# Kernel tuning notes

Measured on AMD Instinct MI355X. Metric: run time of the kernel, lower is better.

Reference implementation:

```python
import jax, jax.numpy as jnp
import numpy as np

N_NODES = 100000
N_EDGES = 1600000
IN_FEATS = 256
OUT_FEATS = 64


def setup_inputs() -> dict:
    key = jax.random.key(0)
    k1, k2, k3, k4 = jax.random.split(key, 4)
    feat = jax.random.normal(k1, (N_NODES, IN_FEATS), dtype=jnp.float32)
    # Glorot uniform init for weight
    limit = float(np.sqrt(6.0 / (IN_FEATS + OUT_FEATS)))
    weight = jax.random.uniform(k2, (IN_FEATS, OUT_FEATS), dtype=jnp.float32,
                                minval=-limit, maxval=limit)
    bias = jnp.zeros((OUT_FEATS,), dtype=jnp.float32)
    src = jax.random.randint(k3, (N_EDGES,), 0, N_NODES, dtype=jnp.int32)
    dst = jax.random.randint(k4, (N_EDGES,), 0, N_NODES, dtype=jnp.int32)
    return {"feat": feat, "weight": weight, "bias": bias, "src": src, "dst": dst}


def reference(feat, weight, bias, src, dst):
    N = feat.shape[0]
    ones = jnp.ones(src.shape[0], dtype=feat.dtype)
    # degrees for symmetric ('both') GCN normalization, clamped to >= 1
    deg_out = jnp.maximum(jax.ops.segment_sum(ones, src, num_segments=N), 1.0)
    deg_in = jnp.maximum(jax.ops.segment_sum(ones, dst, num_segments=N), 1.0)
    norm_out = jax.lax.rsqrt(deg_out)  # [N]
    norm_in = jax.lax.rsqrt(deg_in)    # [N]
    # in_feats > out_feats: project first, then aggregate (forward's taken branch)
    h = jnp.matmul(feat, weight) * norm_out[:, None]          # [N, out]
    agg = jax.ops.segment_sum(h[src], dst, num_segments=N)    # gather+scatter SpMM
    rst = agg * norm_in[:, None] + bias
    return jax.nn.relu(rst)
```

## Files before the change

kernel.cpp:

```cpp
#include <hip/hip_runtime.h>

#define N_NODES 100000
#define N_EDGES 1600000
#define IN_F 256
#define OUT_F 64
#define NPAD 100096
#define NB 391
#define NBLK 512
#define CHUNK 3125
#define MSIZE (2*NB*NBLK)
#define SC_BLOCKS 1564
#define CAP 12288

typedef __attribute__((ext_vector_type(8))) _Float16 half8v;
typedef __attribute__((ext_vector_type(4))) float f32x4;

__device__ __forceinline__ unsigned short f2bf(float f) {
    unsigned u = __builtin_bit_cast(unsigned, f);
    return (unsigned short)((u + 0x7FFFu + ((u >> 16) & 1u)) >> 16);
}
__device__ __forceinline__ float bf2f(unsigned s) {
    return __builtin_bit_cast(float, s << 16);
}
__device__ __forceinline__ half8v cvt8(float4 x, float4 y) {
    half8v r;
    r[0] = (_Float16)x.x; r[1] = (_Float16)x.y; r[2] = (_Float16)x.z; r[3] = (_Float16)x.w;
    r[4] = (_Float16)y.x; r[5] = (_Float16)y.y; r[6] = (_Float16)y.z; r[7] = (_Float16)y.w;
    return r;
}

__global__ __launch_bounds__(256) void histA_kernel(const int* __restrict__ src,
                                                    const int* __restrict__ dst,
                                                    int* __restrict__ hist_g,
                                                    const float* __restrict__ W,
                                                    _Float16* __restrict__ Wt2) {
    __shared__ int hD[NB], hS[NB];
    int b = blockIdx.x, t = threadIdx.x;
    if (b < 64) {
        int i = b * 256 + t;
        int k = i >> 6, c = i & 63;
        int ks4 = k >> 5, kin = k & 31, l4v = kin >> 3, kq = kin & 7;
        int cf  = c >> 4, l15v = c & 15;
        size_t idx = (((size_t)(ks4 * 4 + cf) * 64) + l4v * 16 + l15v) * 8 + kq;
        Wt2[idx] = (_Float16)W[i];
    }
    for (int j = t; j < NB; j += 256) { hD[j] = 0; hS[j] = 0; }
    __syncthreads();
    int e0 = b * CHUNK;
    for (int e = e0 + t; e < e0 + CHUNK; e += 256) {
        atomicAdd(&hD[dst[e] >> 8], 1);
        atomicAdd(&hS[src[e] >> 8], 1);
    }
    __syncthreads();
    for (int j = t; j < NB; j += 256) {
        hist_g[j * NBLK + b] = hD[j];
        hist_g[NB * NBLK + j * NBLK + b] = hS[j];
    }
}

__global__ __launch_bounds__(256) void scan1_kernel(int* __restrict__ data,
                                                    int* __restrict__ partials) {
    __shared__ int sm[256];
    int i = blockIdx.x * 256 + threadIdx.x;
    int v = (i < MSIZE) ? data[i] : 0;
    sm[threadIdx.x] = v;
    __syncthreads();
    int x = v;
    #pragma unroll
    for (int off = 1; off < 256; off <<= 1) {
        int tv = 0;
        if ((int)threadIdx.x >= off) tv = sm[threadIdx.x - off];
        __syncthreads();
        x += tv;
        sm[threadIdx.x] = x;
        __syncthreads();
    }
    if (i < MSIZE) data[i] = x - v;
    if (threadIdx.x == 255) partials[blockIdx.x] = x;
}

__global__ __launch_bounds__(1024) void scan2_kernel(int* __restrict__ partials) {
    __shared__ int sm[1024];
    int i = threadIdx.x;
    int v0 = (2 * i     < SC_BLOCKS) ? partials[2 * i]     : 0;
    int v1 = (2 * i + 1 < SC_BLOCKS) ? partials[2 * i + 1] : 0;
    int pv = v0 + v1;
    sm[i] = pv;
    __syncthreads();
    int x = pv;
    #pragma unroll
    for (int off = 1; off < 1024; off <<= 1) {
        int tv = (i >= off) ? sm[i - off] : 0;
        __syncthreads();
        x += tv;
        sm[i] = x;
        __syncthreads();
    }
    int excl = x - pv;
    if (2 * i     < SC_BLOCKS) partials[2 * i]     = excl;
    if (2 * i + 1 < SC_BLOCKS) partials[2 * i + 1] = excl + v0;
}

__device__ __forceinline__ int gscan(const int* __restrict__ hist_g,
                                     const int* __restrict__ partials, int idx) {
    return hist_g[idx] + partials[idx >> 8];
}

__global__ __launch_bounds__(256) void part_kernel(const int* __restrict__ src,
                                                   const int* __restrict__ dst,
                                                   const int* __restrict__ hist_g,
                                                   const int* __restrict__ partials,
                                                   unsigned* __restrict__ edge_buf,
                                                   int* __restrict__ src_part) {
    __shared__ unsigned stageA[CHUNK], stageB[CHUNK];
    __shared__ unsigned short bkt[CHUNK];
    __shared__ int L[512], cur[512];
    __shared__ int baseD[NB], baseS[NB];
    const int b = blockIdx.x, t = threadIdx.x;
    const int e0 = b * CHUNK;

    for (int j = t; j < NB; j += 256) {
        baseD[j] = gscan(hist_g, partials, j * NBLK + b);
        baseS[j] = gscan(hist_g, partials, NB * NBLK + j * NBLK + b) - N_EDGES;
    }

    L[t] = 0; L[t + 256] = 0;
    __syncthreads();
    for (int i = t; i < CHUNK; i += 256) {
        int d = dst[e0 + i];
        stageA[i] = (unsigned)d;
        atomicAdd(&L[d >> 8], 1);
    }
    __syncthreads();
    int v0 = L[t], v1 = L[t + 256];
    #pragma unroll
    for (int off = 1; off < 512; off <<= 1) {
        int a0 = (t >= off) ? L[t - off] : 0;
        int a1 = (t + 256 >= off) ? L[t + 256 - off] : 0;
        __syncthreads();
        L[t] += a0; L[t + 256] += a1;
        __syncthreads();
    }
    {
        int i0 = L[t], i1 = L[t + 256];
        __syncthreads();
        L[t] = i0 - v0;  L[t + 256] = i1 - v1;
        cur[t] = i0 - v0; cur[t + 256] = i1 - v1;
    }
    __syncthreads();
    for (int i = t; i < CHUNK; i += 256) {
        int d = (int)stageA[i];
        int s = src[e0 + i];
        stageA[i] = (unsigned)s;
        int bj = d >> 8;
        int pos = atomicAdd(&cur[bj], 1);
        stageB[pos] = ((unsigned)(d & 255) << 17) | (unsigned)s;
        bkt[pos] = (unsigned short)bj;
    }
    __syncthreads();
    for (int i = t; i < CHUNK; i += 256) {
        int bj = bkt[i];
        edge_buf[baseD[bj] + (i - L[bj])] = stageB[i];
    }
    __syncthreads();

    L[t] = 0; L[t + 256] = 0;
    __syncthreads();
    for (int i = t; i < CHUNK; i += 256)
        atomicAdd(&L[stageA[i] >> 8], 1);
    __syncthreads();
    v0 = L[t]; v1 = L[t + 256];
    #pragma unroll
    for (int off = 1; off < 512; off <<= 1) {
        int a0 = (t >= off) ? L[t - off] : 0;
        int a1 = (t + 256 >= off) ? L[t + 256 - off] : 0;
        __syncthreads();
        L[t] += a0; L[t + 256] += a1;
        __syncthreads();
    }
    {
        int i0 = L[t], i1 = L[t + 256];
        __syncthreads();
        L[t] = i0 - v0;  L[t + 256] = i1 - v1;
        cur[t] = i0 - v0; cur[t + 256] = i1 - v1;
    }
    __syncthreads();
    for (int i = t; i < CHUNK; i += 256) {
        unsigned s = stageA[i];
        int bj = (int)(s >> 8);
        int pos = atomicAdd(&cur[bj], 1);
        stageB[pos] = s;
        bkt[pos] = (unsigned short)bj;
    }
    __syncthreads();
    for (int i = t; i < CHUNK; i += 256) {
        int bj = bkt[i];
        src_part[baseS[bj] + (i - L[bj])] = (int)stageB[i];
    }
}

__global__ __launch_bounds__(256) void bucket_kernel(unsigned* __restrict__ edge_buf,
                                                     const int* __restrict__ hist_g,
                                                     const int* __restrict__ partials,
                                                     int* __restrict__ row_ptr,
                                                     const int* __restrict__ src_part,
                                                     float* __restrict__ norm_out) {
    __shared__ unsigned stage[CAP];
    __shared__ int hist[256];
    __shared__ int cur[256];
    int j = blockIdx.x, t = threadIdx.x;
    int b0 = gscan(hist_g, partials, j * NBLK);
    int b1 = (j + 1 < NB) ? gscan(hist_g, partials, (j + 1) * NBLK) : N_EDGES;
    int cnt = b1 - b0;
    hist[t] = 0;
    __syncthreads();
    for (int i = t; i < cnt; i += 256) {
        unsigned p = edge_buf[b0 + i];
        stage[i] = p;
        atomicAdd(&hist[p >> 17], 1);
    }
    __syncthreads();
    int v = hist[t];
    cur[t] = v;
    __syncthreads();
    int x = v;
    #pragma unroll
    for (int off = 1; off < 256; off <<= 1) {
        int tv = (t >= off) ? cur[t - off] : 0;
        __syncthreads();
        x += tv;
        cur[t] = x;
        __syncthreads();
    }
    int excl = x - v;
    row_ptr[j * 256 + t] = b0 + excl;
    cur[t] = excl;
    __syncthreads();
    for (int i = t; i < cnt; i += 256) {
        unsigned p = stage[i];
        int pos = atomicAdd(&cur[p >> 17], 1);
        edge_buf[b0 + pos] = p & 0x1FFFFu;
    }
    __syncthreads();
    hist[t] = 0;
    __syncthreads();
    int s0 = gscan(hist_g, partials, NB * NBLK + j * NBLK) - N_EDGES;
    int s1 = (j + 1 < NB) ? gscan(hist_g, partials, NB * NBLK + (j + 1) * NBLK) - N_EDGES
                          : N_EDGES;
    for (int e = s0 + t; e < s1; e += 256)
        atomicAdd(&hist[src_part[e] & 255], 1);
    __syncthreads();
    int node = j * 256 + t;
    if (node < N_NODES) {
        int d = hist[t]; if (d < 1) d = 1;
        norm_out[node] = rsqrtf((float)d);
    }
}

__global__ __launch_bounds__(256) void gemm_kernel(const float* __restrict__ feat,
                                                   const _Float16* __restrict__ Wt2,
                                                   const float* __restrict__ norm_out,
                                                   unsigned short* __restrict__ h) {
    __shared__ _Float16 Bs[16384];
    const int tid  = threadIdx.x;
    const int wave = tid >> 6, lane = tid & 63;
    const int l15  = lane & 15, l4 = lane >> 4;
    const int rw0  = blockIdx.x * 128 + wave * 32;

    #pragma unroll
    for (int i = 0; i < 8; ++i) {
        const int fr = i * 4 + wave;
        const _Float16* gsrc = Wt2 + ((size_t)fr * 64 + lane) * 8;
        _Float16* ldst = &Bs[(size_t)fr * 64 * 8];
        __builtin_amdgcn_global_load_lds(
            (const __attribute__((address_space(1))) void*)gsrc,
            (__attribute__((address_space(3))) void*)ldst, 16, 0, 0);
    }

    int r0 = rw0 + l15;
    int r1 = r0 + 16;
    int r0c = r0 < N_NODES ? r0 : 0;
    int r1c = r1 < N_NODES ? r1 : 0;
    const float* pA0 = feat + (size_t)r0c * IN_F + l4 * 8;
    const float* pA1 = feat + (size_t)r1c * IN_F + l4 * 8;

    f32x4 acc[2][4];
    #pragma unroll
    for (int rf = 0; rf < 2; ++rf)
        #pragma unroll
        for (int cf = 0; cf < 4; ++cf)
            acc[rf][cf] = (f32x4){0.f, 0.f, 0.f, 0.f};

    float4 nx0 = *(const float4*)(pA0);
    float4 ny0 = *(const float4*)(pA0 + 4);
    float4 nx1 = *(const float4*)(pA1);
    float4 ny1 = *(const float4*)(pA1 + 4);

    __syncthreads();

    #pragma unroll
    for (int ks4 = 0; ks4 < 8; ++ks4) {
        float4 cx0 = nx0, cy0 = ny0, cx1 = nx1, cy1 = ny1;
        if (ks4 < 7) {
            nx0 = *(const float4*)(pA0 + 32 * (ks4 + 1));
            ny0 = *(const float4*)(pA0 + 32 * (ks4 + 1) + 4);
            nx1 = *(const float4*)(pA1 + 32 * (ks4 + 1));
            ny1 = *(const float4*)(pA1 + 32 * (ks4 + 1) + 4);
        }
        half8v bfr[4];
        #pragma unroll
        for (int cf = 0; cf < 4; ++cf)
            bfr[cf] = *(const half8v*)&Bs[(((size_t)(ks4 * 4 + cf) * 64) + lane) * 8];
        half8v a0 = cvt8(cx0, cy0);
        half8v a1 = cvt8(cx1, cy1);
        #pragma unroll
        for (int cf = 0; cf < 4; ++cf) {
            acc[0][cf] = __builtin_amdgcn_mfma_f32_16x16x32_f16(a0, bfr[cf], acc[0][cf], 0, 0, 0);
            acc[1][cf] = __builtin_amdgcn_mfma_f32_16x16x32_f16(a1, bfr[cf], acc[1][cf], 0, 0, 0);
        }
    }

    #pragma unroll
    for (int rf = 0; rf < 2; ++rf) {
        #pragma unroll
        for (int r = 0; r < 4; ++r) {
            int row = rw0 + rf * 16 + l4 * 4 + r;
            if (row < N_NODES) {
                float s = norm_out[row];
                #pragma unroll
                for (int cf = 0; cf < 4; ++cf)
                    h[(size_t)row * OUT_F + cf * 16 + l15] = f2bf(acc[rf][cf][r] * s);
            }
        }
    }
}

__global__ __launch_bounds__(256) void agg_kernel(const int* __restrict__ row_ptr,
                                                  const unsigned* __restrict__ edge_src,
                                                  const unsigned short* __restrict__ h,
                                                  const float* __restrict__ bias,
                                                  float* __restrict__ out) {
    int wid  = (blockIdx.x * 256 + threadIdx.x) >> 6;
    int lane = threadIdx.x & 63;
    if (wid >= N_NODES) return;
    int g  = lane >> 3;
    int fp = lane & 7;
    int start = row_ptr[wid];
    int end   = row_ptr[wid + 1];
    int deg   = end - start;

    float a[8];
    #pragma unroll
    for (int i = 0; i < 8; ++i) a[i] = 0.f;

    for (int e = start; e < end; e += 16) {
        int ee0 = e + g, ee1 = e + 8 + g;
        int id0 = (ee0 < end) ? (int)edge_src[ee0] : -1;
        int id1 = (ee1 < end) ? (int)edge_src[ee1] : -1;
        int s0 = id0 >= 0 ? id0 : 0;
        int s1 = id1 >= 0 ? id1 : 0;
        uint4 w0 = *(const uint4*)&h[(size_t)s0 * OUT_F + fp * 8];
        uint4 w1 = *(const uint4*)&h[(size_t)s1 * OUT_F + fp * 8];
        if (id0 < 0) { w0.x = 0u; w0.y = 0u; w0.z = 0u; w0.w = 0u; }
        if (id1 < 0) { w1.x = 0u; w1.y = 0u; w1.z = 0u; w1.w = 0u; }
        a[0] += bf2f(w0.x & 0xFFFFu); a[1] += bf2f(w0.x >> 16);
        a[2] += bf2f(w0.y & 0xFFFFu); a[3] += bf2f(w0.y >> 16);
        a[4] += bf2f(w0.z & 0xFFFFu); a[5] += bf2f(w0.z >> 16);
        a[6] += bf2f(w0.w & 0xFFFFu); a[7] += bf2f(w0.w >> 16);
        a[0] += bf2f(w1.x & 0xFFFFu); a[1] += bf2f(w1.x >> 16);
        a[2] += bf2f(w1.y & 0xFFFFu); a[3] += bf2f(w1.y >> 16);
        a[4] += bf2f(w1.z & 0xFFFFu); a[5] += bf2f(w1.z >> 16);
        a[6] += bf2f(w1.w & 0xFFFFu); a[7] += bf2f(w1.w >> 16);
    }

    #pragma unroll
    for (int off = 8; off < 64; off <<= 1) {
        #pragma unroll
        for (int i = 0; i < 8; ++i) a[i] += __shfl_xor(a[i], off);
    }

    if (g == 0) {
        int dc = deg < 1 ? 1 : deg;
        float nrm = rsqrtf((float)dc);
        float4 b0 = *(const float4*)&bias[fp * 8];
        float4 b1 = *(const float4*)&bias[fp * 8 + 4];
        float4 r0, r1;
        r0.x = fmaxf(a[0] * nrm + b0.x, 0.f);
        r0.y = fmaxf(a[1] * nrm + b0.y, 0.f);
        r0.z = fmaxf(a[2] * nrm + b0.z, 0.f);
        r0.w = fmaxf(a[3] * nrm + b0.w, 0.f);
        r1.x = fmaxf(a[4] * nrm + b1.x, 0.f);
        r1.y = fmaxf(a[5] * nrm + b1.y, 0.f);
        r1.z = fmaxf(a[6] * nrm + b1.z, 0.f);
        r1.w = fmaxf(a[7] * nrm + b1.w, 0.f);
        *(float4*)&out[(size_t)wid * OUT_F + fp * 8]     = r0;
        *(float4*)&out[(size_t)wid * OUT_F + fp * 8 + 4] = r1;
    }
}

extern "C" void kernel_launch(void* const* d_in, const int* in_sizes, int n_in,
                              void* d_out, int out_size, void* d_ws, size_t ws_size,
                              hipStream_t stream) {
    const float* feat = (const float*)d_in[0];
    const float* W    = (const float*)d_in[1];
    const float* bias = (const float*)d_in[2];
    const int*   src  = (const int*)d_in[3];
    const int*   dst  = (const int*)d_in[4];
    float* out = (float*)d_out;

    char* w = (char*)d_ws;
    size_t off = 0;
    auto take = [&](size_t bytes) { char* p = w + off; off += (bytes + 255) & ~(size_t)255; return p; };

    int*            hist_g   = (int*)take((size_t)MSIZE * 4);
    int*            partials = (int*)take((size_t)SC_BLOCKS * 4);
    float*          norm_out = (float*)take((size_t)NPAD * 4);
    int*            row_ptr  = (int*)take((size_t)(NPAD + 64) * 4);
    _Float16*       Wt2      = (_Float16*)take((size_t)IN_F * OUT_F * 2);
    unsigned*       edge_buf = (unsigned*)take((size_t)N_EDGES * 4);
    unsigned short* h        = (unsigned short*)take((size_t)NPAD * OUT_F * 2);
    int*            src_part = (int*)take((size_t)N_EDGES * 4);

    histA_kernel<<<NBLK, 256, 0, stream>>>(src, dst, hist_g, W, Wt2);
    scan1_kernel<<<SC_BLOCKS, 256, 0, stream>>>(hist_g, partials);
    scan2_kernel<<<1, 1024, 0, stream>>>(partials);
    part_kernel<<<NBLK, 256, 0, stream>>>(src, dst, hist_g, partials, edge_buf, src_part);
    bucket_kernel<<<NB, 256, 0, stream>>>(edge_buf, hist_g, partials, row_ptr, src_part, norm_out);
    gemm_kernel<<<(NPAD / 128), 256, 0, stream>>>(feat, Wt2, norm_out, h);
    agg_kernel<<<(N_NODES * 64 + 255) / 256, 256, 0, stream>>>(row_ptr, edge_buf, h, bias, out);
}
```

Baseline: 125.4 us.

## Fuse scan passes via last-block pattern, simplify scatter indexing, unroll aggregation

Removes the separate single-block scan2 launch by having the last scan1 block to finish, detected with an atomic counter and fences, scan the block partials. In part_kernel the per-bucket local offset is folded into the base array, so the scatter loops no longer read L. The aggregation loop now issues four neighbour row gathers per iteration instead of two, giving more loads in flight at the cost of extra registers. The counter is reset inside histA each call, which depends on stream ordering between the two kernels.

Measured after the change: 221.5 us. 76.7% more time.

```diff
diff --git a/kernel.cpp b/kernel.cpp
--- a/kernel.cpp
+++ b/kernel.cpp
@@ -33,9 +33,11 @@
                                                     const int* __restrict__ dst,
                                                     int* __restrict__ hist_g,
                                                     const float* __restrict__ W,
-                                                    _Float16* __restrict__ Wt2) {
+                                                    _Float16* __restrict__ Wt2,
+                                                    int* __restrict__ done) {
     __shared__ int hD[NB], hS[NB];
     int b = blockIdx.x, t = threadIdx.x;
+    if (b == 0 && t == 0) *done = 0;
     if (b < 64) {
         int i = b * 256 + t;
         int k = i >> 6, c = i & 63;
@@ -59,46 +61,64 @@
 }
 
 __global__ __launch_bounds__(256) void scan1_kernel(int* __restrict__ data,
-                                                    int* __restrict__ partials) {
+                                                    int* __restrict__ partials,
+                                                    int* __restrict__ done) {
     __shared__ int sm[256];
-    int i = blockIdx.x * 256 + threadIdx.x;
+    __shared__ int isLast;
+    int t = threadIdx.x;
+    int i = blockIdx.x * 256 + t;
     int v = (i < MSIZE) ? data[i] : 0;
-    sm[threadIdx.x] = v;
+    sm[t] = v;
     __syncthreads();
     int x = v;
     #pragma unroll
     for (int off = 1; off < 256; off <<= 1) {
         int tv = 0;
-        if ((int)threadIdx.x >= off) tv = sm[threadIdx.x - off];
+        if (t >= off) tv = sm[t - off];
         __syncthreads();
         x += tv;
-        sm[threadIdx.x] = x;
+        sm[t] = x;
         __syncthreads();
     }
     if (i < MSIZE) data[i] = x - v;
-    if (threadIdx.x == 255) partials[blockIdx.x] = x;
-}
-
-__global__ __launch_bounds__(1024) void scan2_kernel(int* __restrict__ partials) {
-    __shared__ int sm[1024];
-    int i = threadIdx.x;
-    int v0 = (2 * i     < SC_BLOCKS) ? partials[2 * i]     : 0;
-    int v1 = (2 * i + 1 < SC_BLOCKS) ? partials[2 * i + 1] : 0;
-    int pv = v0 + v1;
-    sm[i] = pv;
-    __syncthreads();
-    int x = pv;
-    #pragma unroll
-    for (int off = 1; off < 1024; off <<= 1) {
-        int tv = (i >= off) ? sm[i - off] : 0;
-        __syncthreads();
-        x += tv;
-        sm[i] = x;
-        __syncthreads();
-    }
-    int excl = x - pv;
-    if (2 * i     < SC_BLOCKS) partials[2 * i]     = excl;
-    if (2 * i + 1 < SC_BLOCKS) partials[2 * i + 1] = excl + v0;
+    if (t == 255) partials[blockIdx.x] = x;
+
+    __threadfence();
+    if (t == 0) {
+        int prev = atomicAdd(done, 1);
+        isLast = (prev == SC_BLOCKS - 1) ? 1 : 0;
+    }
+    __syncthreads();
+    if (isLast) {
+        __threadfence();
+        int base = t * 7;
+        int loc[7];
+        int sum = 0;
+        #pragma unroll
+        for (int q = 0; q < 7; ++q) {
+            int idx = base + q;
+            int pv = (idx < SC_BLOCKS) ? partials[idx] : 0;
+            loc[q] = sum;
+            sum += pv;
+        }
+        sm[t] = sum;
+        __syncthreads();
+        int x2 = sum;
+        #pragma unroll
+        for (int off = 1; off < 256; off <<= 1) {
+            int tv = (t >= off) ? sm[t - off] : 0;
+            __syncthreads();
+            x2 += tv;
+            sm[t] = x2;
+            __syncthreads();
+        }
+        int excl = x2 - sum;
+        #pragma unroll
+        for (int q = 0; q < 7; ++q) {
+            int idx = base + q;
+            if (idx < SC_BLOCKS) partials[idx] = excl + loc[q];
+        }
+    }
 }
 
 __device__ __forceinline__ int gscan(const int* __restrict__ hist_g,
@@ -119,10 +139,10 @@
     const int b = blockIdx.x, t = threadIdx.x;
     const int e0 = b * CHUNK;
 
-    for (int j = t; j < NB; j += 256) {
-        baseD[j] = gscan(hist_g, partials, j * NBLK + b);
-        baseS[j] = gscan(hist_g, partials, NB * NBLK + j * NBLK + b) - N_EDGES;
-    }
+    if (t < NB)       baseD[t]       = gscan(hist_g, partials, t * NBLK + b);
+    if (t + 256 < NB) baseD[t + 256] = gscan(hist_g, partials, (t + 256) * NBLK + b);
+    if (t < NB)       baseS[t]       = gscan(hist_g, partials, NB * NBLK + t * NBLK + b) - N_EDGES;
+    if (t + 256 < NB) baseS[t + 256] = gscan(hist_g, partials, NB * NBLK + (t + 256) * NBLK + b) - N_EDGES;
 
     L[t] = 0; L[t + 256] = 0;
     __syncthreads();
@@ -144,8 +164,11 @@
     {
         int i0 = L[t], i1 = L[t + 256];
         __syncthreads();
-        L[t] = i0 - v0;  L[t + 256] = i1 - v1;
-        cur[t] = i0 - v0; cur[t + 256] = i1 - v1;
+        int e0x = i0 - v0, e1x = i1 - v1;
+        L[t] = e0x;  L[t + 256] = e1x;
+        cur[t] = e0x; cur[t + 256] = e1x;
+        if (t < NB)       baseD[t]       -= e0x;
+        if (t + 256 < NB) baseD[t + 256] -= e1x;
     }
     __syncthreads();
     for (int i = t; i < CHUNK; i += 256) {
@@ -158,10 +181,8 @@
         bkt[pos] = (unsigned short)bj;
     }
     __syncthreads();
-    for (int i = t; i < CHUNK; i += 256) {
-        int bj = bkt[i];
-        edge_buf[baseD[bj] + (i - L[bj])] = stageB[i];
-    }
+    for (int i = t; i < CHUNK; i += 256)
+        edge_buf[baseD[bkt[i]] + i] = stageB[i];
     __syncthreads();
 
     L[t] = 0; L[t + 256] = 0;
@@ -181,8 +202,11 @@
     {
         int i0 = L[t], i1 = L[t + 256];
         __syncthreads();
-        L[t] = i0 - v0;  L[t + 256] = i1 - v1;
-        cur[t] = i0 - v0; cur[t + 256] = i1 - v1;
+        int e0x = i0 - v0, e1x = i1 - v1;
+        L[t] = e0x;  L[t + 256] = e1x;
+        cur[t] = e0x; cur[t + 256] = e1x;
+        if (t < NB)       baseS[t]       -= e0x;
+        if (t + 256 < NB) baseS[t + 256] -= e1x;
     }
     __syncthreads();
     for (int i = t; i < CHUNK; i += 256) {
@@ -193,10 +217,8 @@
         bkt[pos] = (unsigned short)bj;
     }
     __syncthreads();
-    for (int i = t; i < CHUNK; i += 256) {
-        int bj = bkt[i];
-        src_part[baseS[bj] + (i - L[bj])] = (int)stageB[i];
-    }
+    for (int i = t; i < CHUNK; i += 256)
+        src_part[baseS[bkt[i]] + i] = (int)stageB[i];
 }
 
 __global__ __launch_bounds__(256) void bucket_kernel(unsigned* __restrict__ edge_buf,
@@ -353,16 +375,24 @@
     #pragma unroll
     for (int i = 0; i < 8; ++i) a[i] = 0.f;
 
-    for (int e = start; e < end; e += 16) {
-        int ee0 = e + g, ee1 = e + 8 + g;
+    for (int e = start; e < end; e += 32) {
+        int ee0 = e + g, ee1 = ee0 + 8, ee2 = ee0 + 16, ee3 = ee0 + 24;
         int id0 = (ee0 < end) ? (int)edge_src[ee0] : -1;
         int id1 = (ee1 < end) ? (int)edge_src[ee1] : -1;
+        int id2 = (ee2 < end) ? (int)edge_src[ee2] : -1;
+        int id3 = (ee3 < end) ? (int)edge_src[ee3] : -1;
         int s0 = id0 >= 0 ? id0 : 0;
         int s1 = id1 >= 0 ? id1 : 0;
+        int s2 = id2 >= 0 ? id2 : 0;
+        int s3 = id3 >= 0 ? id3 : 0;
         uint4 w0 = *(const uint4*)&h[(size_t)s0 * OUT_F + fp * 8];
         uint4 w1 = *(const uint4*)&h[(size_t)s1 * OUT_F + fp * 8];
+        uint4 w2 = *(const uint4*)&h[(size_t)s2 * OUT_F + fp * 8];
+        uint4 w3 = *(const uint4*)&h[(size_t)s3 * OUT_F + fp * 8];
         if (id0 < 0) { w0.x = 0u; w0.y = 0u; w0.z = 0u; w0.w = 0u; }
         if (id1 < 0) { w1.x = 0u; w1.y = 0u; w1.z = 0u; w1.w = 0u; }
+        if (id2 < 0) { w2.x = 0u; w2.y = 0u; w2.z = 0u; w2.w = 0u; }
+        if (id3 < 0) { w3.x = 0u; w3.y = 0u; w3.z = 0u; w3.w = 0u; }
         a[0] += bf2f(w0.x & 0xFFFFu); a[1] += bf2f(w0.x >> 16);
         a[2] += bf2f(w0.y & 0xFFFFu); a[3] += bf2f(w0.y >> 16);
         a[4] += bf2f(w0.z & 0xFFFFu); a[5] += bf2f(w0.z >> 16);
@@ -371,6 +401,14 @@
         a[2] += bf2f(w1.y & 0xFFFFu); a[3] += bf2f(w1.y >> 16);
         a[4] += bf2f(w1.z & 0xFFFFu); a[5] += bf2f(w1.z >> 16);
         a[6] += bf2f(w1.w & 0xFFFFu); a[7] += bf2f(w1.w >> 16);
+        a[0] += bf2f(w2.x & 0xFFFFu); a[1] += bf2f(w2.x >> 16);
+        a[2] += bf2f(w2.y & 0xFFFFu); a[3] += bf2f(w2.y >> 16);
+        a[4] += bf2f(w2.z & 0xFFFFu); a[5] += bf2f(w2.z >> 16);
+        a[6] += bf2f(w2.w & 0xFFFFu); a[7] += bf2f(w2.w >> 16);
+        a[0] += bf2f(w3.x & 0xFFFFu); a[1] += bf2f(w3.x >> 16);
+        a[2] += bf2f(w3.y & 0xFFFFu); a[3] += bf2f(w3.y >> 16);
+        a[4] += bf2f(w3.z & 0xFFFFu); a[5] += bf2f(w3.z >> 16);
+        a[6] += bf2f(w3.w & 0xFFFFu); a[7] += bf2f(w3.w >> 16);
     }
 
     #pragma unroll
@@ -414,6 +452,7 @@
 
     int*            hist_g   = (int*)take((size_t)MSIZE * 4);
     int*            partials = (int*)take((size_t)SC_BLOCKS * 4);
+    int*            done     = (int*)take(256);
     float*          norm_out = (float*)take((size_t)NPAD * 4);
     int*            row_ptr  = (int*)take((size_t)(NPAD + 64) * 4);
     _Float16*       Wt2      = (_Float16*)take((size_t)IN_F * OUT_F * 2);
@@ -421,9 +460,8 @@
     unsigned short* h        = (unsigned short*)take((size_t)NPAD * OUT_F * 2);
     int*            src_part = (int*)take((size_t)N_EDGES * 4);
 
-    histA_kernel<<<NBLK, 256, 0, stream>>>(src, dst, hist_g, W, Wt2);
-    scan1_kernel<<<SC_BLOCKS, 256, 0, stream>>>(hist_g, partials);
-    scan2_kernel<<<1, 1024, 0, stream>>>(partials);
+    histA_kernel<<<NBLK, 256, 0, stream>>>(src, dst, hist_g, W, Wt2, done);
+    scan1_kernel<<<SC_BLOCKS, 256, 0, stream>>>(hist_g, partials, done);
     part_kernel<<<NBLK, 256, 0, stream>>>(src, dst, hist_g, partials, edge_buf, src_part);
     bucket_kernel<<<NB, 256, 0, stream>>>(edge_buf, hist_g, partials, row_ptr, src_part, norm_out);
     gemm_kernel<<<(NPAD / 128), 256, 0, stream>>>(feat, Wt2, norm_out, h);
```
